# Kernel optimization log

Hardware: AMD Instinct MI355X
Metric: run time of the kernel (lower is better)

The kernel has to match this reference:

```python
import jax, jax.numpy as jnp
import numpy as np

K = 3; STRIDE = 1; PAD = 1; DIL = 1; DG = 1


def _conv(x, w, b):
    y = jax.lax.conv_general_dilated(
        x, w, (STRIDE, STRIDE), [(PAD, PAD), (PAD, PAD)],
        dimension_numbers=("NCHW", "OIHW", "NCHW"))
    return y + b[None, :, None, None]


def _dcnv2(x, offset, mask, w, b):
    # x: [B,C,H,W]; offset: [B,2*DG*K*K,Ho,Wo]; mask: [B,DG*K*K,Ho,Wo] (post-sigmoid)
    B, C, H, W = x.shape
    Ho, Wo = offset.shape[2], offset.shape[3]
    KK = K * K
    Cdg = C // DG
    off = offset.reshape(B, DG, KK, 2, Ho, Wo)
    off_y, off_x = off[:, :, :, 0], off[:, :, :, 1]          # [B,DG,KK,Ho,Wo]
    m = mask.reshape(B, DG, KK, Ho, Wo)
    ky = (jnp.arange(KK) // K) * DIL
    kx = (jnp.arange(KK) % K) * DIL
    base_y = jnp.arange(Ho) * STRIDE - PAD
    base_x = jnp.arange(Wo) * STRIDE - PAD
    py = (base_y[None, :, None] + ky[:, None, None]).astype(x.dtype)  # [KK,Ho,1]
    px = (base_x[None, None, :] + kx[:, None, None]).astype(x.dtype)  # [KK,1,Wo]
    sy = py[None, None] + off_y                               # [B,DG,KK,Ho,Wo]
    sx = px[None, None] + off_x
    y0 = jnp.floor(sy); x0 = jnp.floor(sx)
    wy = sy - y0; wx = sx - x0
    feat = x.reshape(B, DG, Cdg, H * W)

    def corner(iy, ix):
        valid = (iy >= 0) & (iy <= H - 1) & (ix >= 0) & (ix <= W - 1)
        iyc = jnp.clip(iy, 0, H - 1).astype(jnp.int32)
        ixc = jnp.clip(ix, 0, W - 1).astype(jnp.int32)
        idx = (iyc * W + ixc).reshape(B, DG, KK * Ho * Wo)
        g = jax.vmap(jax.vmap(lambda f, i: f[:, i]))(feat, idx)  # [B,DG,Cdg,KK*Ho*Wo]
        g = g.reshape(B, DG, Cdg, KK, Ho, Wo)
        return g * valid[:, :, None].astype(x.dtype)

    one = jnp.asarray(1.0, x.dtype)
    v = (corner(y0, x0) * ((one - wy) * (one - wx))[:, :, None]
         + corner(y0, x0 + 1) * ((one - wy) * wx)[:, :, None]
         + corner(y0 + 1, x0) * (wy * (one - wx))[:, :, None]
         + corner(y0 + 1, x0 + 1) * (wy * wx)[:, :, None])
    v = v * m[:, :, None]                                     # modulation
    wg = w.reshape(w.shape[0], DG, Cdg, KK)                    # [Cout,DG,Cdg,KK]
    out = jnp.einsum("bgckhw,ogck->bohw", v, wg) + b[None, :, None, None]
    return out


def setup_inputs() -> dict:
    key = jax.random.key(0)
    k1, k2, k3 = jax.random.split(key, 3)
    B, C, H, W, Cout = 8, 256, 64, 64, 256
    x = jax.random.normal(k1, (B, C, H, W), jnp.float32)
    w_off = jax.random.normal(k2, (DG * 3 * K * K, C, K, K), jnp.float32) * 0.01
    b_off = jnp.zeros((DG * 3 * K * K,), jnp.float32)
    w_dcn = jax.random.normal(k3, (Cout, C, K, K), jnp.float32) * 0.02
    b_dcn = jnp.zeros((Cout,), jnp.float32)
    return {"x": x, "w_off": w_off, "b_off": b_off, "w_dcn": w_dcn, "b_dcn": b_dcn}


def reference(x, w_off, b_off, w_dcn, b_dcn):
    om = _conv(x, w_off, b_off)                # [B,3*DG*K*K,Ho,Wo]
    o1, o2, mask = jnp.split(om, 3, axis=1)
    offset = jnp.concatenate([o1, o2], axis=1)
    mask = jax.nn.sigmoid(mask)
    return _dcnv2(x, offset, mask, w_dcn, b_dcn)
```

## Files before the change

### kernel.cpp

```cpp
#include <hip/hip_runtime.h>
#include <math.h>

#define BB 8
#define CIN 256
#define HW 4096
#define BHW 32768
#define COUT 256
#define KTOT 2304
#define WS_N (BB*9*HW)

#define WOFF2_OFF (4*WS_N)
#define ACC_OFF   (WOFF2_OFF + 64512)
#define ATOMIC_NEED ((size_t)(ACC_OFF + 27*BHW) * 4)
#define XT_OFF    (ACC_OFF + 27*BHW)
#define NEED3     ((size_t)(XT_OFF + (BB*HW*CIN)/2) * 4)
#define WO16_OFF  (XT_OFF + (BB*HW*CIN)/2)
#define NEED4     ((size_t)(WO16_OFF + 36864) * 4)

#define PQ 520
#define NK2 36

typedef _Float16 hf;
typedef __attribute__((ext_vector_type(8))) _Float16 hfx8;
typedef __attribute__((ext_vector_type(4))) float f32x4;

__global__ __launch_bounds__(256) void prep_kernel(
    const float* __restrict__ x, const float* __restrict__ w_dcn,
    const float* __restrict__ w_off,
    hf* __restrict__ xt, hf* __restrict__ w16, hf* __restrict__ wo16)
{
  __shared__ float t[64][65];
  const int bx = blockIdx.x;
  const int tid = threadIdx.x;

  if (bx < 2048) {
    const int b  = bx >> 8;
    const int cb = (bx & 255) >> 6;
    const int pb = bx & 63;
    const int hi = tid >> 6, lo = tid & 63;
#pragma unroll
    for (int r = 0; r < 16; ++r) {
      int ci = r * 4 + hi;
      t[ci][lo] = x[((size_t)(b * 256 + cb * 64 + ci)) * HW + pb * 64 + lo];
    }
    __syncthreads();
#pragma unroll
    for (int r = 0; r < 16; ++r) {
      int p = r * 4 + hi;
      xt[((size_t)(b * HW + pb * 64 + p)) * 256 + cb * 64 + lo] = (hf)t[lo][p];
    }
  } else if (bx < 2048 + 256) {
    const int co = bx - 2048;
    const int c  = tid;
    const int cblk = c >> 5, cin = c & 31, q = cin >> 3, j = cin & 7;
#pragma unroll
    for (int kk = 0; kk < 9; ++kk)
      w16[(size_t)(cblk * 9 + kk) * 8192 + (q * 256 + co) * 8 + j] =
        (hf)w_dcn[(size_t)co * KTOT + c * 9 + kk];
  } else {
    const int ks = bx - 2304;
    const int cblk = ks / 9, kk = ks - cblk * 9;
    for (int idx = tid; idx < 1024; idx += 256) {
      int lk = idx >> 8, row = (idx >> 3) & 31, j = idx & 7;
      int c = cblk * 32 + lk * 8 + j;
      float v = (row < 27) ? w_off[(size_t)row * KTOT + c * 9 + kk] : 0.f;
      wo16[(size_t)ks * 1024 + idx] = (hf)v;
    }
  }
}

__global__ __launch_bounds__(256) void xpose_kernel(
    const float* __restrict__ x, hf* __restrict__ xt)
{
  __shared__ float t[64][65];
  const int tid = threadIdx.x;
  const int bx  = blockIdx.x;
  const int b   = bx >> 8;
  const int cb  = (bx & 255) >> 6;
  const int pb  = bx & 63;
  const int hi = tid >> 6, lo = tid & 63;
#pragma unroll
  for (int r = 0; r < 16; ++r) {
    int ci = r * 4 + hi;
    t[ci][lo] = x[((size_t)(b * 256 + cb * 64 + ci)) * HW + pb * 64 + lo];
  }
  __syncthreads();
#pragma unroll
  for (int r = 0; r < 16; ++r) {
    int p = r * 4 + hi;
    xt[((size_t)(b * HW + pb * 64 + p)) * 256 + cb * 64 + lo] = (hf)t[lo][p];
  }
}

__global__ __launch_bounds__(256) void wconv_kernel(
    const float* __restrict__ w, hf* __restrict__ o)
{
  const int co = blockIdx.x;
  const int c  = threadIdx.x;
  const int cblk = c >> 5, cin = c & 31, q = cin >> 3, j = cin & 7;
#pragma unroll
  for (int kk = 0; kk < 9; ++kk)
    o[(size_t)(cblk * 9 + kk) * 8192 + (q * 256 + co) * 8 + j] =
      (hf)w[(size_t)co * KTOT + c * 9 + kk];
}

__global__ __launch_bounds__(256) void wprep_kernel(
    const float* __restrict__ w_off, float* __restrict__ woff2)
{
  const int c = blockIdx.x;
  const int tid = threadIdx.x;
  if (tid < 252) {
    int t = tid / 28, j = tid % 28;
    float v = (j < 27) ? w_off[(size_t)j * KTOT + c * 9 + t] : 0.f;
    woff2[((size_t)c * 9 + t) * 28 + j] = v;
  }
}

__global__ __launch_bounds__(256, 2) void offconv_mfma2_kernel(
    const hf* __restrict__ xt, const hf* __restrict__ wo16,
    const float* __restrict__ b_off, float* __restrict__ ws)
{
  __shared__ hf B_lds[2][8 * PQ];
  __shared__ float stage[32][66];

  const int tid  = threadIdx.x;
  const int b    = blockIdx.x & 7;
  const int pos0 = (blockIdx.x >> 3) * 64;

  const int lane = tid & 63, wid = tid >> 6;
  const int lm = lane & 15, lk = lane >> 4;
  const int gp = tid >> 2, gh = tid & 3;
  const int gpos = pos0 + gp;
  const int gho = gpos >> 6, gwo = gpos & 63;

  f32x4 acc[2];
  acc[0] = (f32x4){0.f, 0.f, 0.f, 0.f};
  acc[1] = (f32x4){0.f, 0.f, 0.f, 0.f};

  const hf* bt  = xt + (size_t)b * HW * 256;
  const hf* wga = wo16 + ((lk * 32 + lm) << 3);
  const hfx8 zv = {};

  hfx8 gA, gB;
  bool vA, vB;

#define OG(S, T, CB)                                                     \
  {                                                                      \
    int ky = (T) / 3, kx = (T) - 3 * (ky);                               \
    int yy = gho + ky - 1, xx = gwo + kx - 1;                            \
    v##S = ((unsigned)yy < 64u) && ((unsigned)xx < 64u);                 \
    int row = gpos + (ky - 1) * 64 + (kx - 1);                           \
    row = min(max(row, 0), HW - 1);                                      \
    g##S = *(const hfx8*)(bt + ((size_t)row << 8) + (CB) + gh * 8);      \
  }

  OG(A, 0, 0); OG(B, 1, 0);
  *(hfx8*)&B_lds[0][gh * PQ + gp * 8]       = vA ? gA : zv;
  *(hfx8*)&B_lds[0][(4 + gh) * PQ + gp * 8] = vB ? gB : zv;
  OG(A, 2, 0); OG(B, 3, 0);
  asm volatile("s_waitcnt lgkmcnt(0)" ::: "memory");
  __builtin_amdgcn_sched_barrier(0);
  __builtin_amdgcn_s_barrier();

#pragma unroll 2
  for (int i = 0; i < NK2 - 1; ++i) {
    const int ri = i & 1, wi = ri ^ 1;
    const hf* wg0 = wga + (size_t)(2 * i) * 1024;
    hfx8 af00 = *(const hfx8*)(wg0);
    hfx8 af01 = *(const hfx8*)(wg0 + 128);
    hfx8 af10 = *(const hfx8*)(wg0 + 1024);
    hfx8 af11 = *(const hfx8*)(wg0 + 1024 + 128);

    hfx8 bf0 = *(const hfx8*)&B_lds[ri][lk * PQ + (wid * 16 + lm) * 8];
    hfx8 bf1 = *(const hfx8*)&B_lds[ri][(4 + lk) * PQ + (wid * 16 + lm) * 8];

    *(hfx8*)&B_lds[wi][gh * PQ + gp * 8]       = vA ? gA : zv;
    *(hfx8*)&B_lds[wi][(4 + gh) * PQ + gp * 8] = vB ? gB : zv;

    {
      int ks0 = 2 * i + 4; if (ks0 > 70) ks0 = 70;
      int dA = ks0 / 9; int tA = ks0 - dA * 9; int cbA = dA * 32;
      int ks1 = ks0 + 1;
      int dB = ks1 / 9; int tB = ks1 - dB * 9; int cbB = dB * 32;
      OG(A, tA, cbA); OG(B, tB, cbB);
    }

    acc[0] = __builtin_amdgcn_mfma_f32_16x16x32_f16(af00, bf0, acc[0], 0, 0, 0);
    acc[1] = __builtin_amdgcn_mfma_f32_16x16x32_f16(af01, bf0, acc[1], 0, 0, 0);
    acc[0] = __builtin_amdgcn_mfma_f32_16x16x32_f16(af10, bf1, acc[0], 0, 0, 0);
    acc[1] = __builtin_amdgcn_mfma_f32_16x16x32_f16(af11, bf1, acc[1], 0, 0, 0);

    asm volatile("s_waitcnt lgkmcnt(0)" ::: "memory");
    __builtin_amdgcn_sched_barrier(0);
    __builtin_amdgcn_s_barrier();
  }

  {
    const hf* wg0 = wga + (size_t)70 * 1024;
    hfx8 af00 = *(const hfx8*)(wg0);
    hfx8 af01 = *(const hfx8*)(wg0 + 128);
    hfx8 af10 = *(const hfx8*)(wg0 + 1024);
    hfx8 af11 = *(const hfx8*)(wg0 + 1024 + 128);
    hfx8 bf0 = *(const hfx8*)&B_lds[1][lk * PQ + (wid * 16 + lm) * 8];
    hfx8 bf1 = *(const hfx8*)&B_lds[1][(4 + lk) * PQ + (wid * 16 + lm) * 8];
    acc[0] = __builtin_amdgcn_mfma_f32_16x16x32_f16(af00, bf0, acc[0], 0, 0, 0);
    acc[1] = __builtin_amdgcn_mfma_f32_16x16x32_f16(af01, bf0, acc[1], 0, 0, 0);
    acc[0] = __builtin_amdgcn_mfma_f32_16x16x32_f16(af10, bf1, acc[0], 0, 0, 0);
    acc[1] = __builtin_amdgcn_mfma_f32_16x16x32_f16(af11, bf1, acc[1], 0, 0, 0);
  }

  __syncthreads();
#pragma unroll
  for (int fr = 0; fr < 2; ++fr)
#pragma unroll
    for (int r = 0; r < 4; ++r)
      stage[fr * 16 + lk * 4 + r][wid * 16 + lm] = acc[fr][r];
  __syncthreads();
  for (int t = tid; t < 576; t += 256) {
    int kk = t >> 6, p = t & 63;
    int pos = pos0 + p;
    int ho = pos >> 6, wo = pos & 63;
    float syv = stage[2 * kk][p]     + b_off[2 * kk]     + (float)(ho - 1 + kk / 3);
    float sxv = stage[2 * kk + 1][p] + b_off[2 * kk + 1] + (float)(wo - 1 + kk % 3);
    float mv  = stage[18 + kk][p]    + b_off[18 + kk];
    ws[(b * 9 + kk) * HW + pos]            = syv;
    ws[WS_N + (b * 9 + kk) * HW + pos]     = sxv;
    ws[2 * WS_N + (b * 9 + kk) * HW + pos] = 1.f / (1.f + expf(-mv));
  }
#undef OG
}

template<int NS>
__global__ __launch_bounds__(256) void offconv_atom_kernel(
    const float* __restrict__ x, const float* __restrict__ woff2,
    float* __restrict__ accum)
{
  const int tid = threadIdx.x;
  const int bs  = blockIdx.x;
  const int st  = bs & 15;
  const int b   = (bs >> 4) & 7;
  const int s   = bs >> 7;
  const int pos = st * 256 + tid;
  const int ho  = pos >> 6, wo = pos & 63;
  const int c0  = s * (CIN / NS), c1 = c0 + CIN / NS;

  int   toff[9];
  float tvf[9];
#pragma unroll
  for (int t = 0; t < 9; ++t) {
    int ky = t / 3, kx = t % 3;
    int yy = ho - 1 + ky, xx = wo - 1 + kx;
    bool ok = ((unsigned)yy < 64u) && ((unsigned)xx < 64u);
    toff[t] = (min(max(yy, 0), 63)) * 64 + min(max(xx, 0), 63);
    tvf[t]  = ok ? 1.f : 0.f;
  }
  float a[27];
#pragma unroll
  for (int j = 0; j < 27; ++j) a[j] = 0.f;
  const float* xb = x + (size_t)b * CIN * HW;
#pragma unroll 2
  for (int c = c0; c < c1; ++c) {
    const float* xc = xb + (size_t)c * HW;
    float xv[9];
#pragma unroll
    for (int t = 0; t < 9; ++t) xv[t] = xc[toff[t]] * tvf[t];
    const float4* wr4 = (const float4*)(woff2 + (size_t)c * 252);
#pragma unroll
    for (int t = 0; t < 9; ++t) {
      float4 wb[7];
#pragma unroll
      for (int q = 0; q < 7; ++q) wb[q] = wr4[t * 7 + q];
#pragma unroll
      for (int q = 0; q < 7; ++q) {
        int j0 = q * 4;
        a[j0 + 0] = fmaf(wb[q].x, xv[t], a[j0 + 0]);
        a[j0 + 1] = fmaf(wb[q].y, xv[t], a[j0 + 1]);
        a[j0 + 2] = fmaf(wb[q].z, xv[t], a[j0 + 2]);
        if (j0 + 3 < 27) a[j0 + 3] = fmaf(wb[q].w, xv[t], a[j0 + 3]);
      }
    }
  }
  const int bp = b * HW + pos;
#pragma unroll
  for (int j = 0; j < 27; ++j)
    atomicAdd(&accum[(size_t)j * BHW + bp], a[j]);
}

__global__ __launch_bounds__(256) void combine_kernel(
    const float* __restrict__ b_off, float* __restrict__ ws)
{
  int gid = blockIdx.x * 256 + threadIdx.x;
  int kk = gid >> 15, bp = gid & 32767;
  int b = bp >> 12, pos = bp & 4095;
  int ho = pos >> 6, wo = pos & 63;
  const float* acc = ws + ACC_OFF;
  int jy = 2 * kk, jx = 2 * kk + 1, jm = 18 + kk;
  float syv = acc[(size_t)jy * BHW + bp] + b_off[jy] + (float)(ho - 1 + kk / 3);
  float sxv = acc[(size_t)jx * BHW + bp] + b_off[jx] + (float)(wo - 1 + kk % 3);
  float mv  = acc[(size_t)jm * BHW + bp] + b_off[jm];
  ws[(b * 9 + kk) * HW + pos]            = syv;
  ws[WS_N + (b * 9 + kk) * HW + pos]     = sxv;
  ws[2 * WS_N + (b * 9 + kk) * HW + pos] = 1.f / (1.f + expf(-mv));
}

__global__ __launch_bounds__(256, 2) void dcn_mfma12_kernel(
    const hf* __restrict__ xt, const hf* __restrict__ w16,
    const float* __restrict__ b_dcn, const float* __restrict__ ws,
    float* __restrict__ out)
{
  __shared__ hf B_lds[2][8 * PQ];
  __shared__ int2   pidx[576];
  __shared__ float4 pwts[576];

  const int tid  = threadIdx.x;
  const int b    = blockIdx.x & 7;
  const int pos0 = (blockIdx.x >> 3) * 64;

  for (int t = tid; t < 576; t += 256) {
    int kk = t >> 6, p = t & 63;
    int pos = pos0 + p;
    float sy = ws[(b * 9 + kk) * HW + pos];
    float sx = ws[WS_N + (b * 9 + kk) * HW + pos];
    float m  = ws[2 * WS_N + (b * 9 + kk) * HW + pos];
    float y0f = floorf(sy), x0f = floorf(sx);
    int y0 = (int)y0f, x0 = (int)x0f;
    float wy = sy - y0f, wx = sx - x0f;
    int ix0 = min(max(x0, 0), 63), ix1 = min(max(x0 + 1, 0), 63);
    int bx  = min(max(x0, 0), 62);
    float vx0 = (x0 >= 0  && x0 <= 63) ? 1.f : 0.f;
    float vx1 = (x0 >= -1 && x0 <= 62) ? 1.f : 0.f;
    float wx0 = (1.f - wx) * vx0, wx1 = wx * vx1;
    float a0 = (ix0 == bx     ? wx0 : 0.f) + (ix1 == bx     ? wx1 : 0.f);
    float a1 = (ix0 == bx + 1 ? wx0 : 0.f) + (ix1 == bx + 1 ? wx1 : 0.f);
    int rb0 = min(max(y0, 0), 63), rb1 = min(max(y0 + 1, 0), 63);
    float vy0 = (y0 >= 0  && y0 <= 63) ? 1.f : 0.f;
    float vy1 = (y0 >= -1 && y0 <= 62) ? 1.f : 0.f;
    float wy0m = (1.f - wy) * vy0 * m, wy1m = wy * vy1 * m;
    pidx[t] = make_int2(rb0 * 64 + bx, rb1 * 64 + bx);
    pwts[t] = make_float4(a0 * wy0m, a1 * wy0m, a0 * wy1m, a1 * wy1m);
  }
  __syncthreads();

  const int lane = tid & 63, wid = tid >> 6;
  const int lm = lane & 15, lk = lane >> 4;
  const int chq = tid & 3;
  const int gp  = tid >> 2;

  f32x4 acc[4][4];
#pragma unroll
  for (int a = 0; a < 4; ++a)
#pragma unroll
    for (int c = 0; c < 4; ++c)
      acc[a][c] = (f32x4){0.f, 0.f, 0.f, 0.f};

  const hf* bt  = xt + (size_t)b * HW * 256;
  const hf* wga = w16 + ((lk * 256 + wid * 64 + lm) << 3);
  const int wA = chq * PQ + gp * 8;
  const int wB = (4 + chq) * PQ + gp * 8;

  hf hwA0, hwA1, hwA2, hwA3, hwB0, hwB1, hwB2, hwB3;
  hfx8 cA00, cA01, cA10, cA11, cB00, cB01, cB10, cB11;

#define GATH(S, T, CB)                                                   \
  {                                                                      \
    int pb = (T) * 64 + gp;                                              \
    int2 pi = pidx[pb]; float4 pw = pwts[pb];                            \
    hw##S##0 = (hf)pw.x; hw##S##1 = (hf)pw.y;                            \
    hw##S##2 = (hf)pw.z; hw##S##3 = (hf)pw.w;                            \
    const hf* p0 = bt + ((size_t)pi.x << 8) + (CB) + (chq << 3);         \
    const hf* p1 = bt + ((size_t)pi.y << 8) + (CB) + (chq << 3);         \
    c##S##00 = *(const hfx8*)p0; c##S##01 = *(const hfx8*)(p0 + 256);    \
    c##S##10 = *(const hfx8*)p1; c##S##11 = *(const hfx8*)(p1 + 256);    \
  }

#define COMB(S, DST)                                                     \
  {                                                                      \
    hfx8 vv = c##S##00 * hw##S##0;                                       \
    vv += c##S##01 * hw##S##1;                                           \
    vv += c##S##10 * hw##S##2;                                           \
    vv += c##S##11 * hw##S##3;                                           \
    *(hfx8*)(DST) = vv;                                                  \
  }

  GATH(A, 0, 0); GATH(B, 1, 0);
  COMB(A, &B_lds[0][wA]);
  COMB(B, &B_lds[0][wB]);
  GATH(A, 2, 0); GATH(B, 3, 0);
  asm volatile("s_waitcnt lgkmcnt(0)" ::: "memory");
  __builtin_amdgcn_sched_barrier(0);
  __builtin_amdgcn_s_barrier();

#pragma unroll 2
  for (int i = 0; i < NK2 - 1; ++i) {
    const int ri = i & 1, wi = ri ^ 1;

    const hf* wg0 = wga + (size_t)(2 * i) * 8192;
    hfx8 af0[4], af1[4];
#pragma unroll
    for (int fr = 0; fr < 4; ++fr) af0[fr] = *(const hfx8*)(wg0 + fr * 128);

    hfx8 bf0[4], bf1[4];
#pragma unroll
    for (int pf = 0; pf < 4; ++pf)
      bf0[pf] = *(const hfx8*)&B_lds[ri][lk * PQ + (pf * 16 + lm) * 8];
#pragma unroll
    for (int fr = 0; fr < 4; ++fr) af1[fr] = *(const hfx8*)(wg0 + 8192 + fr * 128);
#pragma unroll
    for (int pf = 0; pf < 4; ++pf)
      bf1[pf] = *(const hfx8*)&B_lds[ri][(4 + lk) * PQ + (pf * 16 + lm) * 8];

    COMB(A, &B_lds[wi][wA]);
    COMB(B, &B_lds[wi][wB]);

    {
      int ks0 = 2 * i + 4; if (ks0 > 70) ks0 = 70;
      int dA = ks0 / 9; int tA = ks0 - dA * 9; int cbA = dA * 32;
      int ks1 = ks0 + 1;
      int dB = ks1 / 9; int tB = ks1 - dB * 9; int cbB = dB * 32;
      GATH(A, tA, cbA); GATH(B, tB, cbB);
    }

#pragma unroll
    for (int fr = 0; fr < 4; ++fr)
#pragma unroll
      for (int pf = 0; pf < 4; ++pf)
        acc[fr][pf] = __builtin_amdgcn_mfma_f32_16x16x32_f16(af0[fr], bf0[pf], acc[fr][pf], 0, 0, 0);
#pragma unroll
    for (int fr = 0; fr < 4; ++fr)
#pragma unroll
      for (int pf = 0; pf < 4; ++pf)
        acc[fr][pf] = __builtin_amdgcn_mfma_f32_16x16x32_f16(af1[fr], bf1[pf], acc[fr][pf], 0, 0, 0);

    asm volatile("s_waitcnt lgkmcnt(0)" ::: "memory");
    __builtin_amdgcn_sched_barrier(0);
    __builtin_amdgcn_s_barrier();
  }

  {
    const hf* wg0 = wga + (size_t)70 * 8192;
    hfx8 af0[4], af1[4];
#pragma unroll
    for (int fr = 0; fr < 4; ++fr) af0[fr] = *(const hfx8*)(wg0 + fr * 128);
#pragma unroll
    for (int fr = 0; fr < 4; ++fr) af1[fr] = *(const hfx8*)(wg0 + 8192 + fr * 128);
    hfx8 bf0[4], bf1[4];
#pragma unroll
    for (int pf = 0; pf < 4; ++pf) {
      bf0[pf] = *(const hfx8*)&B_lds[1][lk * PQ + (pf * 16 + lm) * 8];
      bf1[pf] = *(const hfx8*)&B_lds[1][(4 + lk) * PQ + (pf * 16 + lm) * 8];
    }
#pragma unroll
    for (int fr = 0; fr < 4; ++fr)
#pragma unroll
      for (int pf = 0; pf < 4; ++pf)
        acc[fr][pf] = __builtin_amdgcn_mfma_f32_16x16x32_f16(af0[fr], bf0[pf], acc[fr][pf], 0, 0, 0);
#pragma unroll
    for (int fr = 0; fr < 4; ++fr)
#pragma unroll
      for (int pf = 0; pf < 4; ++pf)
        acc[fr][pf] = __builtin_amdgcn_mfma_f32_16x16x32_f16(af1[fr], bf1[pf], acc[fr][pf], 0, 0, 0);
  }
#undef GATH
#undef COMB

#pragma unroll
  for (int fr = 0; fr < 4; ++fr) {
#pragma unroll
    for (int r = 0; r < 4; ++r) {
      int co = wid * 64 + fr * 16 + lk * 4 + r;
      float bias = b_dcn[co];
      float* orow = out + ((size_t)b * COUT + co) * HW + pos0;
#pragma unroll
      for (int pf = 0; pf < 4; ++pf)
        orow[pf * 16 + lm] = acc[fr][pf][r] + bias;
    }
  }
}

extern "C" void kernel_launch(void* const* d_in, const int* in_sizes, int n_in,
                              void* d_out, int out_size, void* d_ws, size_t ws_size,
                              hipStream_t stream) {
  const float* x     = (const float*)d_in[0];
  const float* w_off = (const float*)d_in[1];
  const float* b_off = (const float*)d_in[2];
  const float* w_dcn = (const float*)d_in[3];
  const float* b_dcn = (const float*)d_in[4];
  float* out = (float*)d_out;
  float* ws  = (float*)d_ws;
  hf* w16  = (hf*)(ws + 3 * WS_N);
  float* woff2 = ws + WOFF2_OFF;

  if (ws_size >= NEED4) {
    hf* xt   = (hf*)(ws + XT_OFF);
    hf* wo16 = (hf*)(ws + WO16_OFF);
    prep_kernel<<<2376, 256, 0, stream>>>(x, w_dcn, w_off, xt, w16, wo16);
    offconv_mfma2_kernel<<<BB * (HW / 64), 256, 0, stream>>>(xt, wo16, b_off, ws);
    dcn_mfma12_kernel<<<BB * (HW / 64), 256, 0, stream>>>(xt, w16, b_dcn, ws, out);
  } else if (ws_size >= NEED3) {
    hf* xt = (hf*)(ws + XT_OFF);
    wconv_kernel<<<COUT, 256, 0, stream>>>(w_dcn, w16);
    wprep_kernel<<<256, 256, 0, stream>>>(w_off, woff2);
    xpose_kernel<<<2048, 256, 0, stream>>>(x, xt);
    hipMemsetAsync(ws + ACC_OFF, 0, (size_t)27 * BHW * 4, stream);
    offconv_atom_kernel<8><<<8 * BB * 16, 256, 0, stream>>>(x, woff2, ws + ACC_OFF);
    combine_kernel<<<(9 * BHW) / 256, 256, 0, stream>>>(b_off, ws);
    dcn_mfma12_kernel<<<BB * (HW / 64), 256, 0, stream>>>(xt, w16, b_dcn, ws, out);
  } else {
    wconv_kernel<<<COUT, 256, 0, stream>>>(w_dcn, w16);
    wprep_kernel<<<256, 256, 0, stream>>>(w_off, woff2);
    hf* xt = (hf*)(ws + ACC_OFF);
    xpose_kernel<<<2048, 256, 0, stream>>>(x, xt);
    offconv_mfma2_kernel<<<BB * (HW / 64), 256, 0, stream>>>(
        xt, (hf*)(ws + ACC_OFF), b_off, ws);
    dcn_mfma12_kernel<<<BB * (HW / 64), 256, 0, stream>>>(xt, w16, b_dcn, ws, out);
  }
}
```

Measured before the change: 87.84 us.

## Fuse offset/mask convolution into deformable conv kernel, drop workspace round trip

Moves the MFMA offset/mask convolution into the prologue of the deformable-conv kernel. Each block computes its 64 positions' offsets and masks in registers and LDS, then builds the bilinear indices and weights directly. This removes a kernel launch and the global write/read of the sy/sx/mask planes, and the fallback workspace paths are simplified. In exchange, each block runs both phases in sequence, which lengthens it and may raise register pressure. In the fallback path, the w16 buffer at ws+3*WS_N may overlap xt placed at ws, so that path could be unsafe.

```diff
diff --git a/kernel.cpp b/kernel.cpp
--- a/kernel.cpp
+++ b/kernel.cpp
@@ -69,244 +69,10 @@
   }
 }
 
-__global__ __launch_bounds__(256) void xpose_kernel(
-    const float* __restrict__ x, hf* __restrict__ xt)
-{
-  __shared__ float t[64][65];
-  const int tid = threadIdx.x;
-  const int bx  = blockIdx.x;
-  const int b   = bx >> 8;
-  const int cb  = (bx & 255) >> 6;
-  const int pb  = bx & 63;
-  const int hi = tid >> 6, lo = tid & 63;
-#pragma unroll
-  for (int r = 0; r < 16; ++r) {
-    int ci = r * 4 + hi;
-    t[ci][lo] = x[((size_t)(b * 256 + cb * 64 + ci)) * HW + pb * 64 + lo];
-  }
-  __syncthreads();
-#pragma unroll
-  for (int r = 0; r < 16; ++r) {
-    int p = r * 4 + hi;
-    xt[((size_t)(b * HW + pb * 64 + p)) * 256 + cb * 64 + lo] = (hf)t[lo][p];
-  }
-}
-
-__global__ __launch_bounds__(256) void wconv_kernel(
-    const float* __restrict__ w, hf* __restrict__ o)
-{
-  const int co = blockIdx.x;
-  const int c  = threadIdx.x;
-  const int cblk = c >> 5, cin = c & 31, q = cin >> 3, j = cin & 7;
-#pragma unroll
-  for (int kk = 0; kk < 9; ++kk)
-    o[(size_t)(cblk * 9 + kk) * 8192 + (q * 256 + co) * 8 + j] =
-      (hf)w[(size_t)co * KTOT + c * 9 + kk];
-}
-
-__global__ __launch_bounds__(256) void wprep_kernel(
-    const float* __restrict__ w_off, float* __restrict__ woff2)
-{
-  const int c = blockIdx.x;
-  const int tid = threadIdx.x;
-  if (tid < 252) {
-    int t = tid / 28, j = tid % 28;
-    float v = (j < 27) ? w_off[(size_t)j * KTOT + c * 9 + t] : 0.f;
-    woff2[((size_t)c * 9 + t) * 28 + j] = v;
-  }
-}
-
-__global__ __launch_bounds__(256, 2) void offconv_mfma2_kernel(
-    const hf* __restrict__ xt, const hf* __restrict__ wo16,
-    const float* __restrict__ b_off, float* __restrict__ ws)
-{
-  __shared__ hf B_lds[2][8 * PQ];
-  __shared__ float stage[32][66];
-
-  const int tid  = threadIdx.x;
-  const int b    = blockIdx.x & 7;
-  const int pos0 = (blockIdx.x >> 3) * 64;
-
-  const int lane = tid & 63, wid = tid >> 6;
-  const int lm = lane & 15, lk = lane >> 4;
-  const int gp = tid >> 2, gh = tid & 3;
-  const int gpos = pos0 + gp;
-  const int gho = gpos >> 6, gwo = gpos & 63;
-
-  f32x4 acc[2];
-  acc[0] = (f32x4){0.f, 0.f, 0.f, 0.f};
-  acc[1] = (f32x4){0.f, 0.f, 0.f, 0.f};
-
-  const hf* bt  = xt + (size_t)b * HW * 256;
-  const hf* wga = wo16 + ((lk * 32 + lm) << 3);
-  const hfx8 zv = {};
-
-  hfx8 gA, gB;
-  bool vA, vB;
-
-#define OG(S, T, CB)                                                     \
-  {                                                                      \
-    int ky = (T) / 3, kx = (T) - 3 * (ky);                               \
-    int yy = gho + ky - 1, xx = gwo + kx - 1;                            \
-    v##S = ((unsigned)yy < 64u) && ((unsigned)xx < 64u);                 \
-    int row = gpos + (ky - 1) * 64 + (kx - 1);                           \
-    row = min(max(row, 0), HW - 1);                                      \
-    g##S = *(const hfx8*)(bt + ((size_t)row << 8) + (CB) + gh * 8);      \
-  }
-
-  OG(A, 0, 0); OG(B, 1, 0);
-  *(hfx8*)&B_lds[0][gh * PQ + gp * 8]       = vA ? gA : zv;
-  *(hfx8*)&B_lds[0][(4 + gh) * PQ + gp * 8] = vB ? gB : zv;
-  OG(A, 2, 0); OG(B, 3, 0);
-  asm volatile("s_waitcnt lgkmcnt(0)" ::: "memory");
-  __builtin_amdgcn_sched_barrier(0);
-  __builtin_amdgcn_s_barrier();
-
-#pragma unroll 2
-  for (int i = 0; i < NK2 - 1; ++i) {
-    const int ri = i & 1, wi = ri ^ 1;
-    const hf* wg0 = wga + (size_t)(2 * i) * 1024;
-    hfx8 af00 = *(const hfx8*)(wg0);
-    hfx8 af01 = *(const hfx8*)(wg0 + 128);
-    hfx8 af10 = *(const hfx8*)(wg0 + 1024);
-    hfx8 af11 = *(const hfx8*)(wg0 + 1024 + 128);
-
-    hfx8 bf0 = *(const hfx8*)&B_lds[ri][lk * PQ + (wid * 16 + lm) * 8];
-    hfx8 bf1 = *(const hfx8*)&B_lds[ri][(4 + lk) * PQ + (wid * 16 + lm) * 8];
-
-    *(hfx8*)&B_lds[wi][gh * PQ + gp * 8]       = vA ? gA : zv;
-    *(hfx8*)&B_lds[wi][(4 + gh) * PQ + gp * 8] = vB ? gB : zv;
-
-    {
-      int ks0 = 2 * i + 4; if (ks0 > 70) ks0 = 70;
-      int dA = ks0 / 9; int tA = ks0 - dA * 9; int cbA = dA * 32;
-      int ks1 = ks0 + 1;
-      int dB = ks1 / 9; int tB = ks1 - dB * 9; int cbB = dB * 32;
-      OG(A, tA, cbA); OG(B, tB, cbB);
-    }
-
-    acc[0] = __builtin_amdgcn_mfma_f32_16x16x32_f16(af00, bf0, acc[0], 0, 0, 0);
-    acc[1] = __builtin_amdgcn_mfma_f32_16x16x32_f16(af01, bf0, acc[1], 0, 0, 0);
-    acc[0] = __builtin_amdgcn_mfma_f32_16x16x32_f16(af10, bf1, acc[0], 0, 0, 0);
-    acc[1] = __builtin_amdgcn_mfma_f32_16x16x32_f16(af11, bf1, acc[1], 0, 0, 0);
-
-    asm volatile("s_waitcnt lgkmcnt(0)" ::: "memory");
-    __builtin_amdgcn_sched_barrier(0);
-    __builtin_amdgcn_s_barrier();
-  }
-
-  {
-    const hf* wg0 = wga + (size_t)70 * 1024;
-    hfx8 af00 = *(const hfx8*)(wg0);
-    hfx8 af01 = *(const hfx8*)(wg0 + 128);
-    hfx8 af10 = *(const hfx8*)(wg0 + 1024);
-    hfx8 af11 = *(const hfx8*)(wg0 + 1024 + 128);
-    hfx8 bf0 = *(const hfx8*)&B_lds[1][lk * PQ + (wid * 16 + lm) * 8];
-    hfx8 bf1 = *(const hfx8*)&B_lds[1][(4 + lk) * PQ + (wid * 16 + lm) * 8];
-    acc[0] = __builtin_amdgcn_mfma_f32_16x16x32_f16(af00, bf0, acc[0], 0, 0, 0);
-    acc[1] = __builtin_amdgcn_mfma_f32_16x16x32_f16(af01, bf0, acc[1], 0, 0, 0);
-    acc[0] = __builtin_amdgcn_mfma_f32_16x16x32_f16(af10, bf1, acc[0], 0, 0, 0);
-    acc[1] = __builtin_amdgcn_mfma_f32_16x16x32_f16(af11, bf1, acc[1], 0, 0, 0);
-  }
-
-  __syncthreads();
-#pragma unroll
-  for (int fr = 0; fr < 2; ++fr)
-#pragma unroll
-    for (int r = 0; r < 4; ++r)
-      stage[fr * 16 + lk * 4 + r][wid * 16 + lm] = acc[fr][r];
-  __syncthreads();
-  for (int t = tid; t < 576; t += 256) {
-    int kk = t >> 6, p = t & 63;
-    int pos = pos0 + p;
-    int ho = pos >> 6, wo = pos & 63;
-    float syv = stage[2 * kk][p]     + b_off[2 * kk]     + (float)(ho - 1 + kk / 3);
-    float sxv = stage[2 * kk + 1][p] + b_off[2 * kk + 1] + (float)(wo - 1 + kk % 3);
-    float mv  = stage[18 + kk][p]    + b_off[18 + kk];
-    ws[(b * 9 + kk) * HW + pos]            = syv;
-    ws[WS_N + (b * 9 + kk) * HW + pos]     = sxv;
-    ws[2 * WS_N + (b * 9 + kk) * HW + pos] = 1.f / (1.f + expf(-mv));
-  }
-#undef OG
-}
-
-template<int NS>
-__global__ __launch_bounds__(256) void offconv_atom_kernel(
-    const float* __restrict__ x, const float* __restrict__ woff2,
-    float* __restrict__ accum)
-{
-  const int tid = threadIdx.x;
-  const int bs  = blockIdx.x;
-  const int st  = bs & 15;
-  const int b   = (bs >> 4) & 7;
-  const int s   = bs >> 7;
-  const int pos = st * 256 + tid;
-  const int ho  = pos >> 6, wo = pos & 63;
-  const int c0  = s * (CIN / NS), c1 = c0 + CIN / NS;
-
-  int   toff[9];
-  float tvf[9];
-#pragma unroll
-  for (int t = 0; t < 9; ++t) {
-    int ky = t / 3, kx = t % 3;
-    int yy = ho - 1 + ky, xx = wo - 1 + kx;
-    bool ok = ((unsigned)yy < 64u) && ((unsigned)xx < 64u);
-    toff[t] = (min(max(yy, 0), 63)) * 64 + min(max(xx, 0), 63);
-    tvf[t]  = ok ? 1.f : 0.f;
-  }
-  float a[27];
-#pragma unroll
-  for (int j = 0; j < 27; ++j) a[j] = 0.f;
-  const float* xb = x + (size_t)b * CIN * HW;
-#pragma unroll 2
-  for (int c = c0; c < c1; ++c) {
-    const float* xc = xb + (size_t)c * HW;
-    float xv[9];
-#pragma unroll
-    for (int t = 0; t < 9; ++t) xv[t] = xc[toff[t]] * tvf[t];
-    const float4* wr4 = (const float4*)(woff2 + (size_t)c * 252);
-#pragma unroll
-    for (int t = 0; t < 9; ++t) {
-      float4 wb[7];
-#pragma unroll
-      for (int q = 0; q < 7; ++q) wb[q] = wr4[t * 7 + q];
-#pragma unroll
-      for (int q = 0; q < 7; ++q) {
-        int j0 = q * 4;
-        a[j0 + 0] = fmaf(wb[q].x, xv[t], a[j0 + 0]);
-        a[j0 + 1] = fmaf(wb[q].y, xv[t], a[j0 + 1]);
-        a[j0 + 2] = fmaf(wb[q].z, xv[t], a[j0 + 2]);
-        if (j0 + 3 < 27) a[j0 + 3] = fmaf(wb[q].w, xv[t], a[j0 + 3]);
-      }
-    }
-  }
-  const int bp = b * HW + pos;
-#pragma unroll
-  for (int j = 0; j < 27; ++j)
-    atomicAdd(&accum[(size_t)j * BHW + bp], a[j]);
-}
-
-__global__ __launch_bounds__(256) void combine_kernel(
-    const float* __restrict__ b_off, float* __restrict__ ws)
-{
-  int gid = blockIdx.x * 256 + threadIdx.x;
-  int kk = gid >> 15, bp = gid & 32767;
-  int b = bp >> 12, pos = bp & 4095;
-  int ho = pos >> 6, wo = pos & 63;
-  const float* acc = ws + ACC_OFF;
-  int jy = 2 * kk, jx = 2 * kk + 1, jm = 18 + kk;
-  float syv = acc[(size_t)jy * BHW + bp] + b_off[jy] + (float)(ho - 1 + kk / 3);
-  float sxv = acc[(size_t)jx * BHW + bp] + b_off[jx] + (float)(wo - 1 + kk % 3);
-  float mv  = acc[(size_t)jm * BHW + bp] + b_off[jm];
-  ws[(b * 9 + kk) * HW + pos]            = syv;
-  ws[WS_N + (b * 9 + kk) * HW + pos]     = sxv;
-  ws[2 * WS_N + (b * 9 + kk) * HW + pos] = 1.f / (1.f + expf(-mv));
-}
-
-__global__ __launch_bounds__(256, 2) void dcn_mfma12_kernel(
+__global__ __launch_bounds__(256, 2) void dcn_fused_kernel(
     const hf* __restrict__ xt, const hf* __restrict__ w16,
-    const float* __restrict__ b_dcn, const float* __restrict__ ws,
-    float* __restrict__ out)
+    const hf* __restrict__ wo16, const float* __restrict__ b_off,
+    const float* __restrict__ b_dcn, float* __restrict__ out)
 {
   __shared__ hf B_lds[2][8 * PQ];
   __shared__ int2   pidx[576];
@@ -316,35 +82,128 @@
   const int b    = blockIdx.x & 7;
   const int pos0 = (blockIdx.x >> 3) * 64;
 
-  for (int t = tid; t < 576; t += 256) {
-    int kk = t >> 6, p = t & 63;
-    int pos = pos0 + p;
-    float sy = ws[(b * 9 + kk) * HW + pos];
-    float sx = ws[WS_N + (b * 9 + kk) * HW + pos];
-    float m  = ws[2 * WS_N + (b * 9 + kk) * HW + pos];
-    float y0f = floorf(sy), x0f = floorf(sx);
-    int y0 = (int)y0f, x0 = (int)x0f;
-    float wy = sy - y0f, wx = sx - x0f;
-    int ix0 = min(max(x0, 0), 63), ix1 = min(max(x0 + 1, 0), 63);
-    int bx  = min(max(x0, 0), 62);
-    float vx0 = (x0 >= 0  && x0 <= 63) ? 1.f : 0.f;
-    float vx1 = (x0 >= -1 && x0 <= 62) ? 1.f : 0.f;
-    float wx0 = (1.f - wx) * vx0, wx1 = wx * vx1;
-    float a0 = (ix0 == bx     ? wx0 : 0.f) + (ix1 == bx     ? wx1 : 0.f);
-    float a1 = (ix0 == bx + 1 ? wx0 : 0.f) + (ix1 == bx + 1 ? wx1 : 0.f);
-    int rb0 = min(max(y0, 0), 63), rb1 = min(max(y0 + 1, 0), 63);
-    float vy0 = (y0 >= 0  && y0 <= 63) ? 1.f : 0.f;
-    float vy1 = (y0 >= -1 && y0 <= 62) ? 1.f : 0.f;
-    float wy0m = (1.f - wy) * vy0 * m, wy1m = wy * vy1 * m;
-    pidx[t] = make_int2(rb0 * 64 + bx, rb1 * 64 + bx);
-    pwts[t] = make_float4(a0 * wy0m, a1 * wy0m, a0 * wy1m, a1 * wy1m);
-  }
-  __syncthreads();
-
   const int lane = tid & 63, wid = tid >> 6;
   const int lm = lane & 15, lk = lane >> 4;
+  const int gp = tid >> 2;
+  const int gh = tid & 3;
+  const int gpos = pos0 + gp;
+  const int gho = gpos >> 6, gwo = gpos & 63;
+
+  const hf* bt = xt + (size_t)b * HW * 256;
+  const hfx8 zv = {};
+
+  {
+    f32x4 oacc[2];
+    oacc[0] = (f32x4){0.f, 0.f, 0.f, 0.f};
+    oacc[1] = (f32x4){0.f, 0.f, 0.f, 0.f};
+    const hf* wga = wo16 + ((lk * 32 + lm) << 3);
+
+    hfx8 gA, gB;
+    bool vA, vB;
+
+#define OG(S, T, CB)                                                     \
+    {                                                                    \
+      int ky = (T) / 3, kx = (T) - 3 * (ky);                             \
+      int yy = gho + ky - 1, xx = gwo + kx - 1;                          \
+      v##S = ((unsigned)yy < 64u) && ((unsigned)xx < 64u);               \
+      int row = gpos + (ky - 1) * 64 + (kx - 1);                         \
+      row = min(max(row, 0), HW - 1);                                    \
+      g##S = *(const hfx8*)(bt + ((size_t)row << 8) + (CB) + gh * 8);    \
+    }
+
+    OG(A, 0, 0); OG(B, 1, 0);
+    *(hfx8*)&B_lds[0][gh * PQ + gp * 8]       = vA ? gA : zv;
+    *(hfx8*)&B_lds[0][(4 + gh) * PQ + gp * 8] = vB ? gB : zv;
+    OG(A, 2, 0); OG(B, 3, 0);
+    asm volatile("s_waitcnt lgkmcnt(0)" ::: "memory");
+    __builtin_amdgcn_sched_barrier(0);
+    __builtin_amdgcn_s_barrier();
+
+#pragma unroll 2
+    for (int i = 0; i < NK2 - 1; ++i) {
+      const int ri = i & 1, wi = ri ^ 1;
+      const hf* wg0 = wga + (size_t)(2 * i) * 1024;
+      hfx8 af00 = *(const hfx8*)(wg0);
+      hfx8 af01 = *(const hfx8*)(wg0 + 128);
+      hfx8 af10 = *(const hfx8*)(wg0 + 1024);
+      hfx8 af11 = *(const hfx8*)(wg0 + 1024 + 128);
+
+      hfx8 bf0 = *(const hfx8*)&B_lds[ri][lk * PQ + (wid * 16 + lm) * 8];
+      hfx8 bf1 = *(const hfx8*)&B_lds[ri][(4 + lk) * PQ + (wid * 16 + lm) * 8];
+
+      *(hfx8*)&B_lds[wi][gh * PQ + gp * 8]       = vA ? gA : zv;
+      *(hfx8*)&B_lds[wi][(4 + gh) * PQ + gp * 8] = vB ? gB : zv;
+
+      {
+        int ks0 = 2 * i + 4; if (ks0 > 70) ks0 = 70;
+        int dA = ks0 / 9; int tA = ks0 - dA * 9; int cbA = dA * 32;
+        int ks1 = ks0 + 1;
+        int dB = ks1 / 9; int tB = ks1 - dB * 9; int cbB = dB * 32;
+        OG(A, tA, cbA); OG(B, tB, cbB);
+      }
+
+      oacc[0] = __builtin_amdgcn_mfma_f32_16x16x32_f16(af00, bf0, oacc[0], 0, 0, 0);
+      oacc[1] = __builtin_amdgcn_mfma_f32_16x16x32_f16(af01, bf0, oacc[1], 0, 0, 0);
+      oacc[0] = __builtin_amdgcn_mfma_f32_16x16x32_f16(af10, bf1, oacc[0], 0, 0, 0);
+      oacc[1] = __builtin_amdgcn_mfma_f32_16x16x32_f16(af11, bf1, oacc[1], 0, 0, 0);
+
+      asm volatile("s_waitcnt lgkmcnt(0)" ::: "memory");
+      __builtin_amdgcn_sched_barrier(0);
+      __builtin_amdgcn_s_barrier();
+    }
+
+    {
+      const hf* wg0 = wga + (size_t)70 * 1024;
+      hfx8 af00 = *(const hfx8*)(wg0);
+      hfx8 af01 = *(const hfx8*)(wg0 + 128);
+      hfx8 af10 = *(const hfx8*)(wg0 + 1024);
+      hfx8 af11 = *(const hfx8*)(wg0 + 1024 + 128);
+      hfx8 bf0 = *(const hfx8*)&B_lds[1][lk * PQ + (wid * 16 + lm) * 8];
+      hfx8 bf1 = *(const hfx8*)&B_lds[1][(4 + lk) * PQ + (wid * 16 + lm) * 8];
+      oacc[0] = __builtin_amdgcn_mfma_f32_16x16x32_f16(af00, bf0, oacc[0], 0, 0, 0);
+      oacc[1] = __builtin_amdgcn_mfma_f32_16x16x32_f16(af01, bf0, oacc[1], 0, 0, 0);
+      oacc[0] = __builtin_amdgcn_mfma_f32_16x16x32_f16(af10, bf1, oacc[0], 0, 0, 0);
+      oacc[1] = __builtin_amdgcn_mfma_f32_16x16x32_f16(af11, bf1, oacc[1], 0, 0, 0);
+    }
+#undef OG
+
+    float* stage = (float*)&B_lds[0][0];
+    __syncthreads();
+#pragma unroll
+    for (int fr = 0; fr < 2; ++fr)
+#pragma unroll
+      for (int r = 0; r < 4; ++r)
+        stage[(fr * 16 + lk * 4 + r) * 66 + wid * 16 + lm] = oacc[fr][r];
+    __syncthreads();
+    for (int t = tid; t < 576; t += 256) {
+      int kk = t >> 6, p = t & 63;
+      int pos = pos0 + p;
+      int ho = pos >> 6, wo = pos & 63;
+      float sy = stage[(2 * kk) * 66 + p]     + b_off[2 * kk]     + (float)(ho - 1 + kk / 3);
+      float sx = stage[(2 * kk + 1) * 66 + p] + b_off[2 * kk + 1] + (float)(wo - 1 + kk % 3);
+      float mv = stage[(18 + kk) * 66 + p]    + b_off[18 + kk];
+      float m  = 1.f / (1.f + expf(-mv));
+      float y0f = floorf(sy), x0f = floorf(sx);
+      int y0 = (int)y0f, x0 = (int)x0f;
+      float wy = sy - y0f, wx = sx - x0f;
+      int ix0 = min(max(x0, 0), 63), ix1 = min(max(x0 + 1, 0), 63);
+      int bx  = min(max(x0, 0), 62);
+      float vx0 = (x0 >= 0  && x0 <= 63) ? 1.f : 0.f;
+      float vx1 = (x0 >= -1 && x0 <= 62) ? 1.f : 0.f;
+      float wx0 = (1.f - wx) * vx0, wx1 = wx * vx1;
+      float a0 = (ix0 == bx     ? wx0 : 0.f) + (ix1 == bx     ? wx1 : 0.f);
+      float a1 = (ix0 == bx + 1 ? wx0 : 0.f) + (ix1 == bx + 1 ? wx1 : 0.f);
+      int rb0 = min(max(y0, 0), 63), rb1 = min(max(y0 + 1, 0), 63);
+      float vy0 = (y0 >= 0  && y0 <= 63) ? 1.f : 0.f;
+      float vy1 = (y0 >= -1 && y0 <= 62) ? 1.f : 0.f;
+      float wy0m = (1.f - wy) * vy0 * m, wy1m = wy * vy1 * m;
+      pidx[t] = make_int2(rb0 * 64 + bx, rb1 * 64 + bx);
+      pwts[t] = make_float4(a0 * wy0m, a1 * wy0m, a0 * wy1m, a1 * wy1m);
+    }
+    __syncthreads();
+  }
+
   const int chq = tid & 3;
-  const int gp  = tid >> 2;
 
   f32x4 acc[4][4];
 #pragma unroll
@@ -353,7 +212,6 @@
     for (int c = 0; c < 4; ++c)
       acc[a][c] = (f32x4){0.f, 0.f, 0.f, 0.f};
 
-  const hf* bt  = xt + (size_t)b * HW * 256;
   const hf* wga = w16 + ((lk * 256 + wid * 64 + lm) << 3);
   const int wA = chq * PQ + gp * 8;
   const int wB = (4 + chq) * PQ + gp * 8;
@@ -488,30 +346,17 @@
   float* out = (float*)d_out;
   float* ws  = (float*)d_ws;
   hf* w16  = (hf*)(ws + 3 * WS_N);
-  float* woff2 = ws + WOFF2_OFF;
-
+
+  hf* xt;
+  hf* wo16;
   if (ws_size >= NEED4) {
-    hf* xt   = (hf*)(ws + XT_OFF);
-    hf* wo16 = (hf*)(ws + WO16_OFF);
-    prep_kernel<<<2376, 256, 0, stream>>>(x, w_dcn, w_off, xt, w16, wo16);
-    offconv_mfma2_kernel<<<BB * (HW / 64), 256, 0, stream>>>(xt, wo16, b_off, ws);
-    dcn_mfma12_kernel<<<BB * (HW / 64), 256, 0, stream>>>(xt, w16, b_dcn, ws, out);
-  } else if (ws_size >= NEED3) {
-    hf* xt = (hf*)(ws + XT_OFF);
-    wconv_kernel<<<COUT, 256, 0, stream>>>(w_dcn, w16);
-    wprep_kernel<<<256, 256, 0, stream>>>(w_off, woff2);
-    xpose_kernel<<<2048, 256, 0, stream>>>(x, xt);
-    hipMemsetAsync(ws + ACC_OFF, 0, (size_t)27 * BHW * 4, stream);
-    offconv_atom_kernel<8><<<8 * BB * 16, 256, 0, stream>>>(x, woff2, ws + ACC_OFF);
-    combine_kernel<<<(9 * BHW) / 256, 256, 0, stream>>>(b_off, ws);
-    dcn_mfma12_kernel<<<BB * (HW / 64), 256, 0, stream>>>(xt, w16, b_dcn, ws, out);
+    xt   = (hf*)(ws + XT_OFF);
+    wo16 = (hf*)(ws + WO16_OFF);
   } else {
-    wconv_kernel<<<COUT, 256, 0, stream>>>(w_dcn, w16);
-    wprep_kernel<<<256, 256, 0, stream>>>(w_off, woff2);
-    hf* xt = (hf*)(ws + ACC_OFF);
-    xpose_kernel<<<2048, 256, 0, stream>>>(x, xt);
-    offconv_mfma2_kernel<<<BB * (HW / 64), 256, 0, stream>>>(
-        xt, (hf*)(ws + ACC_OFF), b_off, ws);
-    dcn_mfma12_kernel<<<BB * (HW / 64), 256, 0, stream>>>(xt, w16, b_dcn, ws, out);
-  }
+    xt   = (hf*)ws;
+    wo16 = (hf*)(ws + (BB * HW * CIN) / 2);
+  }
+
+  prep_kernel<<<2376, 256, 0, stream>>>(x, w_dcn, w_off, xt, w16, wo16);
+  dcn_fused_kernel<<<BB * (HW / 64), 256, 0, stream>>>(xt, w16, wo16, b_off, b_dcn, out);
 }
```

Measured after the change: 82.60 us. -6.0%, faster.
